# Kernel optimization log

Measured on AMD Instinct MI355X. Metric: run time of the kernel, lower is better.

Reference implementation:

```python
import jax, jax.numpy as jnp
import numpy as np

EPS = 1e-5
N_HEADS = 32
TEMPERATURE = 1.0


def _inorm(x, g, b):
    # InstanceNorm2d (affine): normalize over H,W per (N, C)
    m = jnp.mean(x, axis=(-2, -1), keepdims=True)
    v = jnp.var(x, axis=(-2, -1), keepdims=True)
    return (x - m) * jax.lax.rsqrt(v + EPS) * g + b


def _resample(x, out_hw):
    # Fourier (spectral) resampling, matching neuraloperator's resample for skips
    H, W = x.shape[-2:]
    Ho, Wo = out_hw
    if (H, W) == (Ho, Wo):
        return x
    xf = jnp.fft.rfft2(x, norm='forward')
    kh = min(H, Ho) // 2
    kw = min(W // 2 + 1, Wo // 2 + 1)
    of = jnp.zeros(x.shape[:-2] + (Ho, Wo // 2 + 1), dtype=xf.dtype)
    of = of.at[..., :kh, :kw].set(xf[..., :kh, :kw])
    of = of.at[..., -kh:, :kw].set(xf[..., -kh:, :kw])
    return jnp.fft.irfft2(of, s=(Ho, Wo), norm='forward')


def _spec_conv(x, w, out_hw):
    # w: [2(pos/neg rows), in, out, m1, m2, 2(re/im)]; fft_norm='forward'
    m1, m2 = w.shape[3], w.shape[4]
    Ho, Wo = out_hw
    wc = w[..., 0] + 1j * w[..., 1]  # [2, in, out, m1, m2]
    xf = jnp.fft.rfft2(x, norm='forward')  # [B, Cin, H, W//2+1]
    top = jnp.einsum('bimn,iomn->bomn', xf[:, :, :m1, :m2], wc[0])
    bot = jnp.einsum('bimn,iomn->bomn', xf[:, :, -m1:, :m2], wc[1])
    of = jnp.zeros((x.shape[0], w.shape[2], Ho, Wo // 2 + 1), dtype=xf.dtype)
    of = of.at[:, :, :m1, :m2].set(top)
    of = of.at[:, :, -m1:, :m2].set(bot)
    return jnp.fft.irfft2(of, s=(Ho, Wo), norm='forward')


def _fno_layer(x, w, ws, bs, out_hw, norm_gb=None, act=False):
    # one FNOBlock layer: spectral conv + linear (1x1) skip, optional instance norm + gelu
    skip = jnp.einsum('bchw,oc->bohw', x, ws) + bs[None, :, None, None]
    skip = _resample(skip, out_hw)
    fno = _spec_conv(x, w, out_hw)
    if norm_gb is not None:
        fno = _inorm(fno, norm_gb[0], norm_gb[1])
    y = fno + skip
    if act:
        y = jax.nn.gelu(y, approximate=False)  # torch F.gelu default = exact erf
    return y


def _forward(x, wK, wKs, bKs, wQ, wQs, bQs, wV, wVs, bVs, wP, wPs, bPs,
             wM0, wM0s, bM0s, wM1, wM1s, bM1s, norm_g, norm_b):
    B, T, H, W = x.shape  # token_codimension == 1 -> tokens T == channels
    xa = x.reshape(B * T, 1, H, W)
    xa_n = _inorm(xa, norm_g[0], norm_b[0])  # self.norm1
    # K, Q at half resolution (output_scaling_factor = 1/scale, scale = 2); V at full res
    k = _fno_layer(xa_n, wK, wKs, bKs, (H // 2, W // 2))
    q = _fno_layer(xa_n, wQ, wQs, bQs, (H // 2, W // 2))
    v = _fno_layer(xa_n, wV, wVs, bVs, (H, W))

    def to_seq(z):
        h, w = z.shape[-2:]
        z = z.reshape(B, T, N_HEADS, 1, h, w).transpose(0, 2, 1, 3, 4, 5)
        return z.reshape(B, N_HEADS, T, h * w)  # d = head_codim = 1

    qs, ks, vs = to_seq(q), to_seq(k), to_seq(v)
    scores = jnp.einsum('bhtd,bhsd->bhts', qs, ks) / (np.sqrt(ks.shape[-1]).astype(np.float32) * TEMPERATURE)
    attn_w = jax.nn.softmax(scores, axis=-1)
    out = jnp.einsum('bhts,bhsd->bhtd', attn_w, vs)  # [B, heads, T, H*W]
    out = out.reshape(B, N_HEADS, T, 1, H, W).transpose(0, 2, 1, 3, 4, 5)
    out = out.reshape(B * T, N_HEADS, H, W)
    # proj: n_heads*head_codim != token_codim -> FNO projection back to 1 channel
    projd = _fno_layer(out, wP, wPs, bPs, (H, W))
    attention = _inorm(projd + xa, norm_g[1], norm_b[1])  # attention_normalizer
    an = _inorm(attention, norm_g[2], norm_b[2])  # self.norm2
    # permutation-equivariant mixer: 2 FNO layers, instance_norm, gelu between layers
    m = _fno_layer(an, wM0, wM0s, bM0s, (H, W), (norm_g[3], norm_b[3]), act=True)
    m = _fno_layer(m, wM1, wM1s, bM1s, (H, W), (norm_g[4], norm_b[4]), act=False)
    output = _inorm(m, norm_g[5], norm_b[5]) + attention  # mixer_out_normalizer + residual
    return output.reshape(B, T, H, W)


def setup_inputs() -> dict:
    key = jax.random.key(0)
    ks = jax.random.split(key, 16)
    B, T, H, W, heads = 2, 32, 128, 128, 32

    def rn(k, shape, s=1.0):
        return jax.random.normal(k, shape, jnp.float32) * s

    inp = {'x': rn(ks[0], (B, T, H, W))}
    for i, nm in enumerate(['K', 'Q', 'V']):
        inp['w' + nm] = rn(ks[1 + 3 * i], (2, 1, heads, 16, 16, 2), 1.0 / heads)
        inp['w' + nm + 's'] = rn(ks[2 + 3 * i], (heads, 1), 1.0)
        inp['b' + nm + 's'] = jnp.zeros((heads,), jnp.float32)
    inp['wP'] = rn(ks[10], (2, heads, 1, 32, 32, 2), 1.0 / heads)
    inp['wPs'] = rn(ks[11], (1, heads), 1.0 / heads)
    inp['bPs'] = jnp.zeros((1,), jnp.float32)
    inp['wM0'] = rn(ks[12], (2, 1, 1, 32, 32, 2), 1.0)
    inp['wM0s'] = rn(ks[13], (1, 1), 1.0)
    inp['bM0s'] = jnp.zeros((1,), jnp.float32)
    inp['wM1'] = rn(ks[14], (2, 1, 1, 32, 32, 2), 1.0)
    inp['wM1s'] = rn(ks[15], (1, 1), 1.0)
    inp['bM1s'] = jnp.zeros((1,), jnp.float32)
    inp['norm_g'] = jnp.ones((6,), jnp.float32)
    inp['norm_b'] = jnp.zeros((6,), jnp.float32)
    return inp


def reference(x, wK, wKs, bKs, wQ, wQs, bQs, wV, wVs, bVs, wP, wPs, bPs,
              wM0, wM0s, bM0s, wM1, wM1s, bM1s, norm_g, norm_b):
    return _forward(x, wK, wKs, bKs, wQ, wQs, bQs, wV, wVs, bVs, wP, wPs, bPs,
                    wM0, wM0s, bM0s, wM1, wM1s, bM1s, norm_g, norm_b)
```

## Files before the change

kernel.cpp:

```cpp
#include <hip/hip_runtime.h>
#include <math.h>


#define EPSV 1e-5f
#define PI2 6.283185307179586f

typedef float2 cf;

__device__ __forceinline__ cf cmul(cf a, cf b){ return make_float2(a.x*b.x - a.y*b.y, a.x*b.y + a.y*b.x); }
__device__ __forceinline__ cf ldc(const float* p){ return make_float2(p[0], p[1]); }
__device__ __forceinline__ void stc(float* p, cf v){ p[0]=v.x; p[1]=v.y; }

__device__ __forceinline__ void init_tw(cf* tw, int N, float dir){
  for (int j = threadIdx.x; j < N; j += blockDim.x){
    float s, c; sincosf(dir * PI2 * (float)j / (float)N, &s, &c);
    tw[j] = make_float2(c, s);
  }
}

__device__ void breduce2(float& a, float& b){
  __shared__ float sha[16], shb[16];
  for (int off = 32; off > 0; off >>= 1){
    a += __shfl_down(a, off, 64);
    b += __shfl_down(b, off, 64);
  }
  int w = threadIdx.x >> 6, lane = threadIdx.x & 63;
  int nw = (blockDim.x + 63) >> 6;
  if (lane == 0){ sha[w] = a; shb[w] = b; }
  __syncthreads();
  if (threadIdx.x == 0){
    for (int i = 1; i < nw; ++i){ a += sha[i]; b += shb[i]; }
    sha[0] = a; shb[0] = b;
  }
  __syncthreads();
  a = sha[0]; b = shb[0];
  __syncthreads();
}

__device__ __forceinline__ cf kq_mode(const float* w, int o, int kh, int kw){
  if (kw < 16){
    if (kh < 16)  return ldc(w + ((o*16+kh)*16+kw)*2);
    if (kh >= 48) return ldc(w + (((32+o)*16+(kh-48))*16+kw)*2);
  }
  return make_float2(0.f,0.f);
}

__global__ __launch_bounds__(256) void k_gamma_xstats(
                      const float* __restrict__ wQ, const float* __restrict__ wQs,
                      const float* __restrict__ bQs,
                      const float* __restrict__ wK, const float* __restrict__ wKs,
                      const float* __restrict__ bKs,
                      const float* __restrict__ x, const float* __restrict__ ng,
                      const float* __restrict__ nb,
                      float* __restrict__ gam, float* __restrict__ gcons,
                      float* __restrict__ stats, float* __restrict__ normAB){
  if (blockIdx.x >= 32){
    int n = blockIdx.x - 32;
    const float* im = x + n*16384;
    float s=0.f, s2=0.f;
    for (int i=threadIdx.x;i<16384;i+=256){ float v=im[i]; s+=v; s2=fmaf(v,v,s2); }
    breduce2(s,s2);
    if (threadIdx.x==0){
      float m = s*(1.f/16384.f), var = s2*(1.f/16384.f)-m*m;
      float A = rsqrtf(var+EPSV)*ng[0];
      normAB[n*2]=A; normAB[n*2+1]=nb[0]-m*A;
    }
    return;
  }
  int o = blockIdx.x;
  if (o==0){ for (int i=threadIdx.x;i<640;i+=256) stats[i]=0.f; }
  float sQ=wQs[o], sK=wKs[o];
  for (int m = threadIdx.x; m < 2112; m += 256){
    int kh = m/33, kw = m-kh*33;
    cf g;
    if (kw == 0){
      int mh = (64-kh)&63;
      cf qp = kq_mode(wQ,o,kh,0);  qp.x += sQ;
      cf qm = kq_mode(wQ,o,mh,0);  qm.x += sQ;
      cf qt = make_float2(0.5f*(qp.x+qm.x), 0.5f*(qp.y-qm.y));
      cf kp = kq_mode(wK,o,kh,0);  kp.x += sK;
      cf km = kq_mode(wK,o,mh,0);  km.x += sK;
      cf kt = make_float2(0.5f*(kp.x+km.x), 0.5f*(kp.y-km.y));
      g = make_float2(64.f*(qt.x*kt.x + qt.y*kt.y), 64.f*(qt.y*kt.x - qt.x*kt.y));
    } else if (kw == 32){
      g = make_float2(64.f*sQ*sK, 0.f);
    } else {
      cf q = kq_mode(wQ,o,kh,kw); q.x += sQ;
      cf k = kq_mode(wK,o,kh,kw); k.x += sK;
      g = make_float2(128.f*(q.x*k.x + q.y*k.y), 128.f*(q.y*k.x - q.x*k.y));
    }
    stc(gam + (o*2112+m)*2, g);
  }
  if (threadIdx.x == 0){
    float qt0 = sQ + kq_mode(wQ,o,0,0).x;
    float kt0 = sK + kq_mode(wK,o,0,0).x;
    gcons[o]    = 64.f*bKs[o]*qt0;
    gcons[32+o] = 64.f*bQs[o]*kt0;
    gcons[64+o] = 64.f*bQs[o]*bKs[o];
  }
}

__global__ __launch_bounds__(256) void k_rfft_row_x(const float* __restrict__ x, const float* __restrict__ normAB,
                                                    float* __restrict__ Cw){
  __shared__ float tile[16][128];
  __shared__ cf tw[128];
  init_tw(tw, 128, -1.f);
  int n = blockIdx.x, h0 = blockIdx.y*16;
  float A = normAB[n*2], Bc = normAB[n*2+1];
  for (int i=threadIdx.x;i<2048;i+=256) tile[i>>7][i&127] = fmaf(x[n*16384 + h0*128 + i], A, Bc);
  __syncthreads();
  for (int i=threadIdx.x;i<1024;i+=256){
    int hl=i>>6, w=i&63;
    float a=tile[hl][w], b=tile[hl][w+64];
    tile[hl][w]=a+b; tile[hl][w+64]=a-b;
  }
  __syncthreads();
  int hl = threadIdx.x >> 4, kws = threadIdx.x & 15;
  for (int kw=kws; kw<33; kw+=16){
    int sel = (kw&1)? 64 : 0;
    float re=0.f, im=0.f; int idx=0;
    for (int w=0;w<64;++w){
      float v=tile[hl][sel+w]; cf t=tw[idx];
      re=fmaf(v,t.x,re); im=fmaf(v,t.y,im);
      idx=(idx+kw)&127;
    }
    float* d = Cw + (((n*128)+(h0+hl))*33 + kw)*2;
    d[0]=re*(1.f/16384.f); d[1]=im*(1.f/16384.f);
  }
}

__global__ __launch_bounds__(256) void k_fcol(const float* __restrict__ Cw, float* __restrict__ F){
  __shared__ cf col[4][128];
  __shared__ cf tw[128];
  init_tw(tw, 128, -1.f);
  int n = blockIdx.x, kwb = blockIdx.y*4;
  for (int i=threadIdx.x;i<512;i+=256){
    int kwl=i>>7, h=i&127; int kw=kwb+kwl;
    col[kwl][h] = (kw<33) ? ldc(Cw + ((n*128+h)*33+kw)*2) : make_float2(0.f,0.f);
  }
  __syncthreads();
  {
    int i = threadIdx.x;
    int kwl = i>>6, h = i&63;
    cf a = col[kwl][h], b = col[kwl][h+64];
    col[kwl][h]    = make_float2(a.x+b.x, a.y+b.y);
    col[kwl][h+64] = make_float2(a.x-b.x, a.y-b.y);
  }
  __syncthreads();
  int r = threadIdx.x & 63, kwl = threadIdx.x >> 6;
  int kw = kwb + kwl;
  if (kw >= 33) return;
  int R = (r<32)? r : r+64;
  int sel = (r&1)? 64 : 0;
  float re=0.f, im=0.f; int idx=0;
  for (int j=0;j<64;++j){
    cf v=col[kwl][sel+j]; cf t=tw[idx];
    re = fmaf(v.x,t.x,re); re = fmaf(-v.y,t.y,re);
    im = fmaf(v.x,t.y,im); im = fmaf(v.y,t.x,im);
    idx=(idx+R)&127;
  }
  stc(F + ((n*64+r)*33+kw)*2, make_float2(re,im));
}

__global__ __launch_bounds__(256) void k_score(const float* __restrict__ F, const float* __restrict__ gam,
                                               float* __restrict__ scoreP){
  __shared__ float2 Esh[66][33];
  __shared__ float2 gsh[4][66];
  int mk = blockIdx.x, b = blockIdx.y, og = blockIdx.z;
  int m0 = mk*66;
  int t = threadIdx.x >> 3, s4 = (threadIdx.x & 7) << 2;
  for (int i = threadIdx.x; i < 2112; i += 256){
    int tt = i/66, j = i - tt*66;
    int m = m0 + j;
    int kh = m/33, kw = m - kh*33;
    const float* Fb = F + (b*32+tt)*4224;
    float2 v;
    if (kw < 32) v = *(const float2*)(Fb + (kh*33+kw)*2);
    else {
      int mh = (64-kh)&63;
      float2 a = *(const float2*)(Fb + (kh*33+32)*2);
      float2 c = *(const float2*)(Fb + (mh*33+32)*2);
      v = make_float2(0.5f*(a.x+c.x), 0.5f*(a.y-c.y));
    }
    Esh[j][tt] = v;
  }
  for (int i = threadIdx.x; i < 264; i += 256){
    int ol = i/66, j = i - ol*66;
    gsh[ol][j] = *(const float2*)(gam + ((og*4+ol)*2112 + m0 + j)*2);
  }
  __syncthreads();
  float acc[4][4];
  #pragma unroll
  for (int a=0;a<4;++a) for (int k=0;k<4;++k) acc[a][k]=0.f;
  #pragma unroll 2
  for (int j=0;j<66;++j){
    float2 et = Esh[j][t];
    float2 e0 = Esh[j][s4+0];
    float2 e1 = Esh[j][s4+1];
    float2 e2 = Esh[j][s4+2];
    float2 e3 = Esh[j][s4+3];
    #pragma unroll
    for (int ol=0;ol<4;++ol){
      float2 g = gsh[ol][j];
      float a  = g.x*et.x - g.y*et.y;
      float bb = g.x*et.y + g.y*et.x;
      acc[ol][0] = fmaf(a,e0.x,fmaf(bb,e0.y,acc[ol][0]));
      acc[ol][1] = fmaf(a,e1.x,fmaf(bb,e1.y,acc[ol][1]));
      acc[ol][2] = fmaf(a,e2.x,fmaf(bb,e2.y,acc[ol][2]));
      acc[ol][3] = fmaf(a,e3.x,fmaf(bb,e3.y,acc[ol][3]));
    }
  }
  #pragma unroll
  for (int ol=0;ol<4;++ol){
    int o = og*4+ol;
    float* sp = scoreP + (((mk*2+b)*32+o)*32 + t)*32 + s4;
    sp[0]=acc[ol][0]; sp[1]=acc[ol][1]; sp[2]=acc[ol][2]; sp[3]=acc[ol][3];
  }
}

__global__ __launch_bounds__(1024) void k_softmax(float* __restrict__ attn, const float* __restrict__ F,
                                                const float* __restrict__ gcons, const float* __restrict__ scoreP){
  __shared__ float Ssh[32][33];
  int b = blockIdx.x, o = blockIdx.y;
  int t = threadIdx.x >> 5, s = threadIdx.x & 31;
  float c0=gcons[o], c1=gcons[32+o], c2=gcons[64+o];
  float sc = c0*F[(b*32+t)*4224] + c1*F[(b*32+s)*4224] + c2;
  #pragma unroll 8
  for (int p=0;p<32;++p) sc += scoreP[(((p*2+b)*32+o)*32 + t)*32 + s];
  Ssh[t][s] = sc;
  __syncthreads();
  float mx = -1e30f;
  for (int ss=0;ss<32;++ss) mx = fmaxf(mx, Ssh[t][ss]);
  float e = expf(sc - mx);
  __syncthreads();
  Ssh[t][s] = e;
  __syncthreads();
  float sum = 0.f;
  for (int ss=0;ss<32;++ss) sum += Ssh[t][ss];
  attn[(b*32+o)*1024 + t*32 + s] = e/sum;
}

__device__ __forceinline__ cf wcV_col0(const float* wV, int o, int fr){
  if (fr < 16)  return ldc(wV + ((o*16+fr)*16)*2);
  if (fr >= 112) return ldc(wV + (((32+o)*16+(fr-112))*16)*2);
  return make_float2(0.f,0.f);
}

__global__ __launch_bounds__(256) void k_pmode(const float* __restrict__ F, const float* __restrict__ attn,
                        const float* __restrict__ wV, const float* __restrict__ wVs,
                        const float* __restrict__ wP, const float* __restrict__ wPs,
                        float* __restrict__ Pm){
  __shared__ float att[32][8][32];
  __shared__ cf Fsh[32][32];
  __shared__ cf dsh[32][32];
  int b = blockIdx.x, mh = blockIdx.y, tg = blockIdx.z;
  int fr = mh<32 ? mh : mh+64;
  int half = (mh>=32)?1:0, mr = mh&31;
  for (int i=threadIdx.x; i<8192; i+=256){
    int o = i>>8, r = i&255;
    att[o][r>>5][r&31] = attn[(b*32+o)*1024 + tg*256 + r];
  }
  for (int i=threadIdx.x; i<1024; i+=256){
    int s=i>>5, kw=i&31;
    Fsh[s][kw] = ldc(F + (((b*32+s)*64+mh)*33+kw)*2);
  }
  for (int i=threadIdx.x; i<1024; i+=256){
    int o=i>>5, kw=i&31;
    cf wp = ldc(wP + (((half*32+o)*32+mr)*32+kw)*2);
    cf bP = make_float2(wPs[o]+wp.x, wp.y);
    cf aV = make_float2(wVs[o], 0.f);
    if (kw==0){
      cf w1 = wcV_col0(wV,o,fr);
      cf w2 = wcV_col0(wV,o,(128-fr)&127);
      aV.x += 0.5f*(w1.x + w2.x);
      aV.y += 0.5f*(w1.y - w2.y);
    } else if (kw<16){
      if (fr<16){ cf wv=ldc(wV + ((o*16+fr)*16+kw)*2); aV.x+=wv.x; aV.y+=wv.y; }
      else if (fr>=112){ cf wv=ldc(wV + (((32+o)*16+(fr-112))*16+kw)*2); aV.x+=wv.x; aV.y+=wv.y; }
    }
    cf c = cmul(bP, aV);
    c.x -= wPs[o]*wVs[o];
    dsh[o][kw]=c;
  }
  __syncthreads();
  int tl = threadIdx.x>>5, kw = threadIdx.x&31;
  float ax=0.f, ay=0.f;
  for (int o=0;o<32;++o){
    float er=0.f, ei=0.f;
    #pragma unroll
    for (int s4=0;s4<32;s4+=4){
      float4 a4 = *(const float4*)&att[o][tl][s4];
      cf f0=Fsh[s4][kw], f1=Fsh[s4+1][kw], f2=Fsh[s4+2][kw], f3=Fsh[s4+3][kw];
      er=fmaf(a4.x,f0.x,er); ei=fmaf(a4.x,f0.y,ei);
      er=fmaf(a4.y,f1.x,er); ei=fmaf(a4.y,f1.y,ei);
      er=fmaf(a4.z,f2.x,er); ei=fmaf(a4.z,f2.y,ei);
      er=fmaf(a4.w,f3.x,er); ei=fmaf(a4.w,f3.y,ei);
    }
    cf d = dsh[o][kw];
    ax += d.x*er - d.y*ei;
    ay += d.x*ei + d.y*er;
  }
  int t = tg*8+tl;
  stc(Pm + ((b*32+t)*2048 + mh*32+kw)*2, make_float2(ax,ay));
}

__global__ __launch_bounds__(256) void k_zmix(const float* __restrict__ x, const float* __restrict__ Pm,
                        const float* __restrict__ attn, const float* __restrict__ normAB,
                        const float* __restrict__ wVs, const float* __restrict__ wPs,
                        const float* __restrict__ wP, const float* __restrict__ bPs,
                        const float* __restrict__ bVs,
                        float* __restrict__ z, float* __restrict__ stats,
                        float* __restrict__ Tm){
  __shared__ cf Pmsh[64][33];
  __shared__ cf PmAsh[16][33];
  __shared__ float zrows[16][128];
  __shared__ float Mrow[32];
  __shared__ float cpart[33];
  __shared__ float consts;
  __shared__ cf tw[128];
  init_tw(tw, 128, 1.f);
  int n = blockIdx.x, b = n>>5, t = n&31, hb = blockIdx.y*8;
  for (int i=threadIdx.x;i<2048;i+=256)
    Pmsh[i>>5][i&31] = ldc(Pm + (n*2048 + i)*2);
  if (threadIdx.x < 32){
    int s = threadIdx.x;
    float a=0.f;
    for (int o=0;o<32;++o) a = fmaf(attn[(b*32+o)*1024 + t*32 + s], wVs[o]*wPs[o], a);
    float AxS = normAB[(b*32+s)*2], BcS = normAB[(b*32+s)*2+1];
    Mrow[s] = fmaf(a, AxS, (s==t)?1.f:0.f);
    cpart[s] = a*BcS;
  } else if (threadIdx.x == 32){
    float dcx = bPs[0];
    for (int o=0;o<32;++o){
      cf wp = ldc(wP + (o*1024)*2);
      dcx += (wPs[o]+wp.x)*bVs[o];
    }
    cpart[32] = dcx;
  }
  __syncthreads();
  if (threadIdx.x == 0){
    float c=0.f;
    for (int i=0;i<33;++i) c += cpart[i];
    consts = c;
  }
  {
    int bl = threadIdx.x>>5, kw = threadIdx.x&31;
    int h = hb + bl;
    float ser=0.f, sei=0.f, sor=0.f, soi=0.f;
    int s2h = (2*h)&127;
    int idx = 0;
    for (int khi=0;khi<32;khi+=2){
      cf v=Pmsh[khi][kw]; cf tt=tw[idx];
      ser += v.x*tt.x - v.y*tt.y; sei += v.x*tt.y + v.y*tt.x;
      idx=(idx+s2h)&127;
    }
    idx = (96*h)&127;
    for (int khi=32;khi<64;khi+=2){
      cf v=Pmsh[khi][kw]; cf tt=tw[idx];
      ser += v.x*tt.x - v.y*tt.y; sei += v.x*tt.y + v.y*tt.x;
      idx=(idx+s2h)&127;
    }
    idx = h&127;
    for (int khi=1;khi<32;khi+=2){
      cf v=Pmsh[khi][kw]; cf tt=tw[idx];
      sor += v.x*tt.x - v.y*tt.y; soi += v.x*tt.y + v.y*tt.x;
      idx=(idx+s2h)&127;
    }
    idx = (97*h)&127;
    for (int khi=33;khi<64;khi+=2){
      cf v=Pmsh[khi][kw]; cf tt=tw[idx];
      sor += v.x*tt.x - v.y*tt.y; soi += v.x*tt.y + v.y*tt.x;
      idx=(idx+s2h)&127;
    }
    PmAsh[bl][kw]   = make_float2(ser+sor, sei+soi);
    PmAsh[8+bl][kw] = make_float2(ser-sor, sei-soi);
  }
  __syncthreads();
  float cst = consts;
  float s1=0.f, s2=0.f;
  const float* xb = x + b*32*16384;
  {
    int hl = threadIdx.x>>4, wg = threadIdx.x&15;
    int w0 = wg*4;
    int gh = (hl<8)? hb+hl : hb+(hl-8)+64;
    int off = gh*128;
    float Se[4], So[4];
    #pragma unroll
    for (int j=0;j<4;++j){
      int w = w0+j;
      int s2w = (2*w)&127;
      float se=0.f, so=0.f;
      int idx=0;
      for (int kwp=0;kwp<16;++kwp){
        cf v = PmAsh[hl][2*kwp]; cf tt=tw[idx];
        float term = v.x*tt.x - v.y*tt.y;
        se += (kwp? 2.f:1.f)*term;
        idx=(idx+s2w)&127;
      }
      idx = w&127;
      for (int kwp=0;kwp<16;++kwp){
        cf v = PmAsh[hl][2*kwp+1]; cf tt=tw[idx];
        so += 2.f*(v.x*tt.x - v.y*tt.y);
        idx=(idx+s2w)&127;
      }
      Se[j]=se; So[j]=so;
    }
    float mixa[4]={0,0,0,0}, mixb[4]={0,0,0,0};
    for (int s=0;s<32;++s){
      float m = Mrow[s];
      float4 xa = *(const float4*)(xb + s*16384 + off + w0);
      float4 xc = *(const float4*)(xb + s*16384 + off + w0 + 64);
      mixa[0]=fmaf(m,xa.x,mixa[0]); mixa[1]=fmaf(m,xa.y,mixa[1]);
      mixa[2]=fmaf(m,xa.z,mixa[2]); mixa[3]=fmaf(m,xa.w,mixa[3]);
      mixb[0]=fmaf(m,xc.x,mixb[0]); mixb[1]=fmaf(m,xc.y,mixb[1]);
      mixb[2]=fmaf(m,xc.z,mixb[2]); mixb[3]=fmaf(m,xc.w,mixb[3]);
    }
    float oa[4], ob[4];
    #pragma unroll
    for (int j=0;j<4;++j){
      oa[j] = cst + Se[j] + So[j] + mixa[j];
      ob[j] = cst + Se[j] - So[j] + mixb[j];
      s1 += oa[j]+ob[j];
      s2 += oa[j]*oa[j] + ob[j]*ob[j];
      zrows[hl][w0+j]    = oa[j];
      zrows[hl][w0+64+j] = ob[j];
    }
    *(float4*)(z + n*16384 + off + w0)      = make_float4(oa[0],oa[1],oa[2],oa[3]);
    *(float4*)(z + n*16384 + off + w0 + 64) = make_float4(ob[0],ob[1],ob[2],ob[3]);
  }
  __syncthreads();
  for (int i=threadIdx.x;i<1024;i+=256){
    int hl=i>>6, w=i&63;
    float a=zrows[hl][w], bz=zrows[hl][w+64];
    zrows[hl][w]=a+bz; zrows[hl][w+64]=a-bz;
  }
  __syncthreads();
  for (int i=threadIdx.x;i<512;i+=256){
    int hl=i>>5, kw=i&31;
    int gh = (hl<8)? hb+hl : hb+(hl-8)+64;
    int sel = (kw&1)? 64 : 0;
    float re=0.f, im=0.f; int idx=0;
    for (int w=0;w<64;++w){
      float v=zrows[hl][sel+w]; cf tt=tw[idx];
      re=fmaf(v,tt.x,re); im=fmaf(v,tt.y,im);
      idx=(idx+kw)&127;
    }
    float* d = Tm + ((n*128+gh)*32+kw)*2;
    d[0]=re*(1.f/16384.f); d[1]=-im*(1.f/16384.f);
  }
  breduce2(s1,s2);
  if (threadIdx.x==0){ atomicAdd(&stats[n*2],s1); atomicAdd(&stats[n*2+1],s2); }
}

__global__ __launch_bounds__(256) void k_colpair(const float* __restrict__ Tm, const float* __restrict__ wM,
                                                 const float* __restrict__ statsZ,
                                                 const float* __restrict__ ng, const float* __restrict__ nb,
                                                 int apply_an, float* __restrict__ Am){
  __shared__ cf Tsh[128][9];
  __shared__ cf Gsh[64][9];
  __shared__ cf tw[128];
  init_tw(tw,128,-1.f);
  int n = blockIdx.x, kw8 = blockIdx.y*8;
  float C1 = 1.f, Dc128 = 0.f;
  if (apply_an){
    float S=statsZ[n*2], S2=statsZ[n*2+1];
    float mz=S*(1.f/16384.f), vz=S2*(1.f/16384.f)-mz*mz;
    float az=rsqrtf(vz+EPSV);
    float g1=ng[1], g2=ng[2];
    float vat = g1*g1*vz*az*az;
    C1 = az*g1*rsqrtf(vat+EPSV)*g2;
    Dc128 = (nb[2] - mz*C1)*(1.f/128.f);
  }
  for (int i=threadIdx.x;i<1024;i+=256){
    int h=i>>3, kwl=i&7;
    cf v = ldc(Tm + ((n*128+h)*32 + kw8+kwl)*2);
    v.x *= C1; v.y *= C1;
    if (apply_an && (kw8+kwl)==0) v.x += Dc128;
    Tsh[h][kwl] = v;
  }
  __syncthreads();
  for (int i=threadIdx.x;i<512;i+=256){
    int h=i>>3, kwl=i&7;
    cf a=Tsh[h][kwl], b=Tsh[h+64][kwl];
    Tsh[h][kwl]    = make_float2(a.x+b.x, a.y+b.y);
    Tsh[h+64][kwl] = make_float2(a.x-b.x, a.y-b.y);
  }
  __syncthreads();
  {
    int kwl = threadIdx.x&7, base = threadIdx.x>>3;
    for (int r=0;r<2;++r){
      int khi = r*32 + base;
      int khF = (khi<32)? khi : khi+64;
      int sel = (khi&1)? 64 : 0;
      float re=0.f, im=0.f; int idx=0;
      for (int j=0;j<64;++j){
        cf v=Tsh[sel+j][kwl]; cf t=tw[idx];
        re += v.x*t.x - v.y*t.y; im += v.x*t.y + v.y*t.x;
        idx=(idx+khF)&127;
      }
      int half=(khi>=32)?1:0, mr=khi&31;
      cf wv = ldc(wM + ((half*32+mr)*32 + kw8+kwl)*2);
      Gsh[khi][kwl] = cmul(make_float2(re,im), wv);
    }
  }
  __syncthreads();
  {
    int kwl = threadIdx.x&7, base = threadIdx.x>>3;
    for (int r=0;r<2;++r){
      int h = r*32 + base;
      float ser=0.f, sei=0.f, sor=0.f, soi=0.f;
      int s2h = (2*h)&127;
      int idx=0;
      for (int khi=0;khi<32;khi+=2){
        cf v=Gsh[khi][kwl]; cf t=tw[idx];
        ser += v.x*t.x + v.y*t.y; sei += v.y*t.x - v.x*t.y;
        idx=(idx+s2h)&127;
      }
      idx=(96*h)&127;
      for (int khi=32;khi<64;khi+=2){
        cf v=Gsh[khi][kwl]; cf t=tw[idx];
        ser += v.x*t.x + v.y*t.y; sei += v.y*t.x - v.x*t.y;
        idx=(idx+s2h)&127;
      }
      idx=h&127;
      for (int khi=1;khi<32;khi+=2){
        cf v=Gsh[khi][kwl]; cf t=tw[idx];
        sor += v.x*t.x + v.y*t.y; soi += v.y*t.x - v.x*t.y;
        idx=(idx+s2h)&127;
      }
      idx=(97*h)&127;
      for (int khi=33;khi<64;khi+=2){
        cf v=Gsh[khi][kwl]; cf t=tw[idx];
        sor += v.x*t.x + v.y*t.y; soi += v.y*t.x - v.x*t.y;
        idx=(idx+s2h)&127;
      }
      stc(Am + ((n*128+h)*32 + kw8+kwl)*2,    make_float2(ser+sor, sei+soi));
      stc(Am + ((n*128+h+64)*32 + kw8+kwl)*2, make_float2(ser-sor, sei-soi));
    }
  }
}

__global__ __launch_bounds__(256) void k_mirfft_row(const float* __restrict__ Am, float* __restrict__ out,
                                                    float* __restrict__ stats,
                                                    const float* __restrict__ m0, float* __restrict__ statsC,
                                                    int withCross){
  __shared__ cf rowA[16][33];
  __shared__ cf tw[128];
  init_tw(tw,128,1.f);
  int n=blockIdx.x, h0=blockIdx.y*16;
  for (int i=threadIdx.x;i<512;i+=256){
    int hl=i>>5, kw=i&31;
    rowA[hl][kw] = ldc(Am + ((n*128+h0+hl)*32+kw)*2);
  }
  __syncthreads();
  float s=0.f,s2=0.f,s3=0.f;
  for (int i=threadIdx.x;i<1024;i+=256){
    int hl=i>>6, w=i&63;
    int s2w = (2*w)&127;
    float se=0.f, so=0.f;
    int idx=0;
    for (int kwp=0;kwp<16;++kwp){
      cf v=rowA[hl][2*kwp]; cf t=tw[idx];
      float term=v.x*t.x-v.y*t.y;
      se += (kwp? 2.f:1.f)*term;
      idx=(idx+s2w)&127;
    }
    idx = w&127;
    for (int kwp=0;kwp<16;++kwp){
      cf v=rowA[hl][2*kwp+1]; cf t=tw[idx];
      so += 2.f*(v.x*t.x-v.y*t.y);
      idx=(idx+s2w)&127;
    }
    float oa = se+so, ob = se-so;
    int gi = n*16384+(h0+hl)*128+w;
    out[gi]    = oa;
    out[gi+64] = ob;
    s+=oa+ob; s2 += oa*oa + ob*ob;
    if (withCross){
      s3 = fmaf(oa, m0[gi], s3);
      s3 = fmaf(ob, m0[gi+64], s3);
    }
  }
  breduce2(s,s2);
  if (threadIdx.x==0){ atomicAdd(&stats[n*2],s); atomicAdd(&stats[n*2+1],s2); }
  if (withCross){
    float d=0.f;
    breduce2(s3,d);
    if (threadIdx.x==0) atomicAdd(&statsC[n*2],s3);
  }
}

__global__ __launch_bounds__(256) void k_m0_rfft_row(const float* __restrict__ fno, const float* __restrict__ z,
                              const float* __restrict__ stats0, const float* __restrict__ statsZ,
                              const float* __restrict__ ng, const float* __restrict__ nb,
                              const float* __restrict__ wM0s, const float* __restrict__ bM0s,
                              float* __restrict__ m0out, float* __restrict__ Tm,
                              float* __restrict__ statsM0){
  __shared__ float tile[16][128];
  __shared__ cf tw[128];
  init_tw(tw,128,-1.f);
  int n=blockIdx.x, h0=blockIdx.y*16;
  float S0=stats0[n*2], S02=stats0[n*2+1];
  float m0m=S0*(1.f/16384.f), v0=S02*(1.f/16384.f)-m0m*m0m;
  float A0=rsqrtf(v0+EPSV)*ng[3];
  float B0=nb[3]-m0m*A0;
  float Sz=statsZ[n*2], Sz2=statsZ[n*2+1];
  float mz=Sz*(1.f/16384.f), vz=Sz2*(1.f/16384.f)-mz*mz;
  float az=rsqrtf(vz+EPSV);
  float g1=ng[1], g2=ng[2];
  float vat=g1*g1*vz*az*az;
  float C1=az*g1*rsqrtf(vat+EPSV)*g2;
  float Dc=nb[2]-mz*C1;
  float ws_=wM0s[0], bs_=bM0s[0];
  float sm=0.f, sm2=0.f;
  for (int i=threadIdx.x;i<2048;i+=256){
    int gi = n*16384 + h0*128 + i;
    float nf = fmaf(fno[gi], A0, B0);
    float an = fmaf(z[gi], C1, Dc);
    float pre = nf + fmaf(ws_, an, bs_);
    float gv = 0.5f*pre*(1.f+erff(pre*0.70710678118654752f));
    tile[i>>7][i&127]=gv;
    m0out[gi]=gv;
    sm+=gv; sm2=fmaf(gv,gv,sm2);
  }
  __syncthreads();
  for (int i=threadIdx.x;i<1024;i+=256){
    int hl=i>>6, w=i&63;
    float a=tile[hl][w], b=tile[hl][w+64];
    tile[hl][w]=a+b; tile[hl][w+64]=a-b;
  }
  __syncthreads();
  for (int i=threadIdx.x;i<512;i+=256){
    int hl=i>>5, kw=i&31;
    int sel = (kw&1)? 64:0;
    float re=0.f,im=0.f; int idx=0;
    for (int w=0;w<64;++w){
      float v=tile[hl][sel+w]; cf t=tw[idx];
      re=fmaf(v,t.x,re); im=fmaf(v,t.y,im);
      idx=(idx+kw)&127;
    }
    float* d = Tm + ((n*128+h0+hl)*32+kw)*2;
    d[0]=re*(1.f/16384.f); d[1]=im*(1.f/16384.f);
  }
  breduce2(sm,sm2);
  if (threadIdx.x==0){ atomicAdd(&statsM0[n*2],sm); atomicAdd(&statsM0[n*2+1],sm2); }
}

__global__ __launch_bounds__(256) void k_final(const float* __restrict__ f1, const float* __restrict__ m0,
                        const float* __restrict__ z,
                        const float* __restrict__ stats1, const float* __restrict__ statsM0,
                        const float* __restrict__ statsC, const float* __restrict__ statsZ,
                        const float* __restrict__ ng, const float* __restrict__ nb,
                        const float* __restrict__ wM1s, const float* __restrict__ bM1s,
                        float* __restrict__ out){
  int n=blockIdx.x, h0=blockIdx.y*16;
  const float N = 16384.f, iN = 1.f/16384.f;
  float Sf=stats1[n*2], Sf2=stats1[n*2+1];
  float m1m=Sf*iN, v1=Sf2*iN-m1m*m1m;
  float A1=rsqrtf(v1+EPSV)*ng[4];
  float Bc1=nb[4]-m1m*A1;
  float ws_=wM1s[0], K=Bc1+bM1s[0];
  float Sm=statsM0[n*2], Sm2=statsM0[n*2+1], Sfm=statsC[n*2];
  float S1m = A1*Sf + ws_*Sm + N*K;
  float S2m = A1*A1*Sf2 + ws_*ws_*Sm2 + N*K*K + 2.f*A1*ws_*Sfm + 2.f*A1*K*Sf + 2.f*ws_*K*Sm;
  float mean2 = S1m*iN, var2 = S2m*iN - mean2*mean2;
  float A2=rsqrtf(var2+EPSV)*ng[5];
  float B2c=nb[5]-mean2*A2;
  float Sz=statsZ[n*2], Sz2=statsZ[n*2+1];
  float mz=Sz*iN, vz=Sz2*iN-mz*mz;
  float Az=rsqrtf(vz+EPSV)*ng[1];
  float Bz=nb[1]-mz*Az;
  float cf1 = A2*A1, cm0 = A2*ws_, cc = A2*K + B2c;
  for (int i=threadIdx.x;i<2048;i+=256){
    int gi=n*16384+h0*128+i;
    out[gi] = fmaf(f1[gi],cf1, fmaf(m0[gi],cm0, cc)) + fmaf(z[gi],Az,Bz);
  }
}

extern "C" void kernel_launch(void* const* d_in, const int* in_sizes, int n_in,
                              void* d_out, int out_size, void* d_ws, size_t ws_size,
                              hipStream_t stream){
  (void)in_sizes; (void)n_in; (void)out_size; (void)ws_size;
  const float* x   = (const float*)d_in[0];
  const float* wK  = (const float*)d_in[1];
  const float* wKs = (const float*)d_in[2];
  const float* bKs = (const float*)d_in[3];
  const float* wQ  = (const float*)d_in[4];
  const float* wQs = (const float*)d_in[5];
  const float* bQs = (const float*)d_in[6];
  const float* wV  = (const float*)d_in[7];
  const float* wVs = (const float*)d_in[8];
  const float* bVs = (const float*)d_in[9];
  const float* wP  = (const float*)d_in[10];
  const float* wPs = (const float*)d_in[11];
  const float* bPs = (const float*)d_in[12];
  const float* wM0 = (const float*)d_in[13];
  const float* wM0s= (const float*)d_in[14];
  const float* bM0s= (const float*)d_in[15];
  const float* wM1 = (const float*)d_in[16];
  const float* wM1s= (const float*)d_in[17];
  const float* bM1s= (const float*)d_in[18];
  const float* ng  = (const float*)d_in[19];
  const float* nb  = (const float*)d_in[20];
  float* out = (float*)d_out;
  float* ws  = (float*)d_ws;

  float* F      = ws;
  float* Cw     = F + 270336;
  float* scoreP = Cw + 540672;
  float* attn   = scoreP + 2097152;
  float* stats  = attn + 65536;
  float* Pm     = stats + 640;
  float* gcons  = Pm + 262144;
  float* gam    = gcons + 128;
  float* normAB = gam + 135168;
  float* z      = normAB + 128;
  float* m0b    = z + 1048576;
  float* fx     = m0b + 1048576;
  float* Tm     = fx + 1048576;
  float* Am     = Tm + 524288;
  float* statsZ = stats;
  float* stats0 = stats + 128;
  float* stats1 = stats + 256;
  float* statsM0= stats + 384;
  float* statsC = stats + 512;

  k_gamma_xstats<<<96,256,0,stream>>>(wQ,wQs,bQs, wK,wKs,bKs, x, ng, nb, gam, gcons, stats, normAB);
  k_rfft_row_x<<<dim3(64,8),256,0,stream>>>(x, normAB, Cw);
  k_fcol<<<dim3(64,9),256,0,stream>>>(Cw, F);
  k_score<<<dim3(32,2,8),256,0,stream>>>(F, gam, scoreP);
  k_softmax<<<dim3(2,32),1024,0,stream>>>(attn, F, gcons, scoreP);
  k_pmode<<<dim3(2,64,4),256,0,stream>>>(F, attn, wV, wVs, wP, wPs, Pm);
  k_zmix<<<dim3(64,8),256,0,stream>>>(x, Pm, attn, normAB, wVs, wPs, wP, bPs, bVs, z, statsZ, Tm);
  k_colpair<<<dim3(64,4),256,0,stream>>>(Tm, wM0, statsZ, ng, nb, 1, Am);
  k_mirfft_row<<<dim3(64,8),256,0,stream>>>(Am, fx, stats0, (const float*)nullptr, (float*)nullptr, 0);
  k_m0_rfft_row<<<dim3(64,8),256,0,stream>>>(fx, z, stats0, statsZ, ng, nb, wM0s, bM0s, m0b, Tm, statsM0);
  k_colpair<<<dim3(64,4),256,0,stream>>>(Tm, wM1, statsZ, ng, nb, 0, Am);
  k_mirfft_row<<<dim3(64,8),256,0,stream>>>(Am, fx, stats1, m0b, statsC, 1);
  k_final<<<dim3(64,8),256,0,stream>>>(fx, m0b, z, stats1, statsM0, statsC, statsZ, ng, nb, wM1s, bM1s, out);
}
```

Before: 250.7 us.

## Compute norm stats in spectral domain and fuse inverse row FFTs into consumers

The spatial-domain sum and sum-of-squares (plus the cross term) needed for instance norm are now computed from the spectral coefficients inside k_colpair using Parseval's identity. That removes the need to materialize the inverse-FFT output before the stats are known. The inverse row DFT is then fused into the GELU/m0 kernel and into the final combine kernel, cutting two launches and one full-size intermediate buffer round-trip. The cost is extra Parseval bookkeeping with subtle edge cases (DC and Nyquist columns, mirrored rows), and the sign convention of Tm's imaginary part changes, which makes correctness fragile.

After: 235.4 us, median of 2. 1.07x faster.

```diff
diff --git a/kernel.cpp b/kernel.cpp
--- a/kernel.cpp
+++ b/kernel.cpp
@@ -455,9 +455,12 @@
 __global__ __launch_bounds__(256) void k_colpair(const float* __restrict__ Tm, const float* __restrict__ wM,
                                                  const float* __restrict__ statsZ,
                                                  const float* __restrict__ ng, const float* __restrict__ nb,
-                                                 int apply_an, float* __restrict__ Am){
+                                                 int apply_an, float* __restrict__ Am,
+                                                 float* __restrict__ statsF,
+                                                 float* __restrict__ statsC, int do_cross){
   __shared__ cf Tsh[128][9];
   __shared__ cf Gsh[64][9];
+  __shared__ cf Msh[64][9];
   __shared__ cf tw[128];
   init_tw(tw,128,-1.f);
   int n = blockIdx.x, kw8 = blockIdx.y*8;
@@ -500,6 +503,7 @@
       }
       int half=(khi>=32)?1:0, mr=khi&31;
       cf wv = ldc(wM + ((half*32+mr)*32 + kw8+kwl)*2);
+      Msh[khi][kwl] = make_float2(re,im);
       Gsh[khi][kwl] = cmul(make_float2(re,im), wv);
     }
   }
@@ -538,13 +542,60 @@
       stc(Am + ((n*128+h+64)*32 + kw8+kwl)*2, make_float2(ser-sor, sei-soi));
     }
   }
-}
-
-__global__ __launch_bounds__(256) void k_mirfft_row(const float* __restrict__ Am, float* __restrict__ out,
-                                                    float* __restrict__ stats,
-                                                    const float* __restrict__ m0, float* __restrict__ statsC,
-                                                    int withCross){
+  float p2=0.f, cx=0.f;
+  for (int i=threadIdx.x;i<512;i+=256){
+    int khi=i>>3, kwl=i&7;
+    int kw=kw8+kwl;
+    if (kw>=1){
+      cf g=Gsh[khi][kwl];
+      p2 += 2.f*(g.x*g.x+g.y*g.y);
+      if (do_cross){ cf m=Msh[khi][kwl]; cx += 2.f*(g.x*m.x+g.y*m.y); }
+    }
+  }
+  if (kw8==0){
+    int tid=threadIdx.x;
+    if (tid==0){
+      cf g0=Gsh[0][0];
+      p2 += g0.x*g0.x;
+      if (do_cross) cx += g0.x*Msh[0][0].x;
+      atomicAdd(&statsF[n*2], 16384.f*g0.x);
+    } else if (tid<32){
+      cf a=Gsh[tid][0], b=Gsh[64-tid][0];
+      float fex=0.5f*(a.x+b.x), fey=0.5f*(a.y-b.y);
+      p2 += 2.f*(fex*fex+fey*fey);
+      if (do_cross){ cf m=Msh[tid][0]; cx += 2.f*(fex*m.x+fey*m.y); }
+    } else if (tid==32){
+      cf v=Gsh[32][0];
+      p2 += 0.5f*(v.x*v.x+v.y*v.y);
+      if (do_cross){
+        float mr=0.f, mi=0.f;
+        for (int j=0;j<64;++j){
+          cf u=Tsh[j][0];
+          int q=j&3;
+          if (q==0){ mr+=u.x; mi+=u.y; }
+          else if (q==1){ mr+=u.y; mi-=u.x; }
+          else if (q==2){ mr-=u.x; mi-=u.y; }
+          else        { mr-=u.y; mi+=u.x; }
+        }
+        cx += v.x*mr + v.y*mi;
+      }
+    }
+  }
+  breduce2(p2,cx);
+  if (threadIdx.x==0){
+    atomicAdd(&statsF[n*2+1], 16384.f*p2);
+    if (do_cross) atomicAdd(&statsC[n*2], 16384.f*cx);
+  }
+}
+
+__global__ __launch_bounds__(256) void k_m0_irow(const float* __restrict__ Am, const float* __restrict__ z,
+                              const float* __restrict__ stats0, const float* __restrict__ statsZ,
+                              const float* __restrict__ ng, const float* __restrict__ nb,
+                              const float* __restrict__ wM0s, const float* __restrict__ bM0s,
+                              float* __restrict__ m0out, float* __restrict__ Tm,
+                              float* __restrict__ statsM0){
   __shared__ cf rowA[16][33];
+  __shared__ float tile[16][128];
   __shared__ cf tw[128];
   init_tw(tw,128,1.f);
   int n=blockIdx.x, h0=blockIdx.y*16;
@@ -552,54 +603,6 @@
     int hl=i>>5, kw=i&31;
     rowA[hl][kw] = ldc(Am + ((n*128+h0+hl)*32+kw)*2);
   }
-  __syncthreads();
-  float s=0.f,s2=0.f,s3=0.f;
-  for (int i=threadIdx.x;i<1024;i+=256){
-    int hl=i>>6, w=i&63;
-    int s2w = (2*w)&127;
-    float se=0.f, so=0.f;
-    int idx=0;
-    for (int kwp=0;kwp<16;++kwp){
-      cf v=rowA[hl][2*kwp]; cf t=tw[idx];
-      float term=v.x*t.x-v.y*t.y;
-      se += (kwp? 2.f:1.f)*term;
-      idx=(idx+s2w)&127;
-    }
-    idx = w&127;
-    for (int kwp=0;kwp<16;++kwp){
-      cf v=rowA[hl][2*kwp+1]; cf t=tw[idx];
-      so += 2.f*(v.x*t.x-v.y*t.y);
-      idx=(idx+s2w)&127;
-    }
-    float oa = se+so, ob = se-so;
-    int gi = n*16384+(h0+hl)*128+w;
-    out[gi]    = oa;
-    out[gi+64] = ob;
-    s+=oa+ob; s2 += oa*oa + ob*ob;
-    if (withCross){
-      s3 = fmaf(oa, m0[gi], s3);
-      s3 = fmaf(ob, m0[gi+64], s3);
-    }
-  }
-  breduce2(s,s2);
-  if (threadIdx.x==0){ atomicAdd(&stats[n*2],s); atomicAdd(&stats[n*2+1],s2); }
-  if (withCross){
-    float d=0.f;
-    breduce2(s3,d);
-    if (threadIdx.x==0) atomicAdd(&statsC[n*2],s3);
-  }
-}
-
-__global__ __launch_bounds__(256) void k_m0_rfft_row(const float* __restrict__ fno, const float* __restrict__ z,
-                              const float* __restrict__ stats0, const float* __restrict__ statsZ,
-                              const float* __restrict__ ng, const float* __restrict__ nb,
-                              const float* __restrict__ wM0s, const float* __restrict__ bM0s,
-                              float* __restrict__ m0out, float* __restrict__ Tm,
-                              float* __restrict__ statsM0){
-  __shared__ float tile[16][128];
-  __shared__ cf tw[128];
-  init_tw(tw,128,-1.f);
-  int n=blockIdx.x, h0=blockIdx.y*16;
   float S0=stats0[n*2], S02=stats0[n*2+1];
   float m0m=S0*(1.f/16384.f), v0=S02*(1.f/16384.f)-m0m*m0m;
   float A0=rsqrtf(v0+EPSV)*ng[3];
@@ -612,16 +615,36 @@
   float C1=az*g1*rsqrtf(vat+EPSV)*g2;
   float Dc=nb[2]-mz*C1;
   float ws_=wM0s[0], bs_=bM0s[0];
+  __syncthreads();
   float sm=0.f, sm2=0.f;
-  for (int i=threadIdx.x;i<2048;i+=256){
-    int gi = n*16384 + h0*128 + i;
-    float nf = fmaf(fno[gi], A0, B0);
-    float an = fmaf(z[gi], C1, Dc);
-    float pre = nf + fmaf(ws_, an, bs_);
-    float gv = 0.5f*pre*(1.f+erff(pre*0.70710678118654752f));
-    tile[i>>7][i&127]=gv;
-    m0out[gi]=gv;
-    sm+=gv; sm2=fmaf(gv,gv,sm2);
+  for (int i=threadIdx.x;i<1024;i+=256){
+    int hl=i>>6, w=i&63;
+    int s2w = (2*w)&127;
+    float se=0.f, so=0.f;
+    int idx=0;
+    for (int kwp=0;kwp<16;++kwp){
+      cf v=rowA[hl][2*kwp]; cf t=tw[idx];
+      float term=v.x*t.x-v.y*t.y;
+      se += (kwp? 2.f:1.f)*term;
+      idx=(idx+s2w)&127;
+    }
+    idx = w&127;
+    for (int kwp=0;kwp<16;++kwp){
+      cf v=rowA[hl][2*kwp+1]; cf t=tw[idx];
+      so += 2.f*(v.x*t.x-v.y*t.y);
+      idx=(idx+s2w)&127;
+    }
+    float oa = se+so, ob = se-so;
+    int gi = n*16384+(h0+hl)*128+w;
+    float an_a = fmaf(z[gi],C1,Dc);
+    float pre_a = fmaf(oa,A0,B0) + fmaf(ws_,an_a,bs_);
+    float ga = 0.5f*pre_a*(1.f+erff(pre_a*0.70710678118654752f));
+    m0out[gi]=ga; tile[hl][w]=ga;
+    float an_b = fmaf(z[gi+64],C1,Dc);
+    float pre_b = fmaf(ob,A0,B0) + fmaf(ws_,an_b,bs_);
+    float gb = 0.5f*pre_b*(1.f+erff(pre_b*0.70710678118654752f));
+    m0out[gi+64]=gb; tile[hl][w+64]=gb;
+    sm += ga+gb; sm2 += ga*ga + gb*gb;
   }
   __syncthreads();
   for (int i=threadIdx.x;i<1024;i+=256){
@@ -640,20 +663,27 @@
       idx=(idx+kw)&127;
     }
     float* d = Tm + ((n*128+h0+hl)*32+kw)*2;
-    d[0]=re*(1.f/16384.f); d[1]=im*(1.f/16384.f);
+    d[0]=re*(1.f/16384.f); d[1]=-im*(1.f/16384.f);
   }
   breduce2(sm,sm2);
   if (threadIdx.x==0){ atomicAdd(&statsM0[n*2],sm); atomicAdd(&statsM0[n*2+1],sm2); }
 }
 
-__global__ __launch_bounds__(256) void k_final(const float* __restrict__ f1, const float* __restrict__ m0,
+__global__ __launch_bounds__(256) void k_final_irow(const float* __restrict__ Am, const float* __restrict__ m0,
                         const float* __restrict__ z,
                         const float* __restrict__ stats1, const float* __restrict__ statsM0,
                         const float* __restrict__ statsC, const float* __restrict__ statsZ,
                         const float* __restrict__ ng, const float* __restrict__ nb,
                         const float* __restrict__ wM1s, const float* __restrict__ bM1s,
                         float* __restrict__ out){
+  __shared__ cf rowA[16][33];
+  __shared__ cf tw[128];
+  init_tw(tw,128,1.f);
   int n=blockIdx.x, h0=blockIdx.y*16;
+  for (int i=threadIdx.x;i<512;i+=256){
+    int hl=i>>5, kw=i&31;
+    rowA[hl][kw] = ldc(Am + ((n*128+h0+hl)*32+kw)*2);
+  }
   const float N = 16384.f, iN = 1.f/16384.f;
   float Sf=stats1[n*2], Sf2=stats1[n*2+1];
   float m1m=Sf*iN, v1=Sf2*iN-m1m*m1m;
@@ -671,9 +701,28 @@
   float Az=rsqrtf(vz+EPSV)*ng[1];
   float Bz=nb[1]-mz*Az;
   float cf1 = A2*A1, cm0 = A2*ws_, cc = A2*K + B2c;
-  for (int i=threadIdx.x;i<2048;i+=256){
-    int gi=n*16384+h0*128+i;
-    out[gi] = fmaf(f1[gi],cf1, fmaf(m0[gi],cm0, cc)) + fmaf(z[gi],Az,Bz);
+  __syncthreads();
+  for (int i=threadIdx.x;i<1024;i+=256){
+    int hl=i>>6, w=i&63;
+    int s2w = (2*w)&127;
+    float se=0.f, so=0.f;
+    int idx=0;
+    for (int kwp=0;kwp<16;++kwp){
+      cf v=rowA[hl][2*kwp]; cf t=tw[idx];
+      float term=v.x*t.x-v.y*t.y;
+      se += (kwp? 2.f:1.f)*term;
+      idx=(idx+s2w)&127;
+    }
+    idx = w&127;
+    for (int kwp=0;kwp<16;++kwp){
+      cf v=rowA[hl][2*kwp+1]; cf t=tw[idx];
+      so += 2.f*(v.x*t.x-v.y*t.y);
+      idx=(idx+s2w)&127;
+    }
+    float oa = se+so, ob = se-so;
+    int gi = n*16384+(h0+hl)*128+w;
+    out[gi]    = fmaf(oa,cf1, fmaf(m0[gi],cm0, cc)) + fmaf(z[gi],Az,Bz);
+    out[gi+64] = fmaf(ob,cf1, fmaf(m0[gi+64],cm0, cc)) + fmaf(z[gi+64],Az,Bz);
   }
 }
 
@@ -716,8 +765,7 @@
   float* normAB = gam + 135168;
   float* z      = normAB + 128;
   float* m0b    = z + 1048576;
-  float* fx     = m0b + 1048576;
-  float* Tm     = fx + 1048576;
+  float* Tm     = m0b + 1048576;
   float* Am     = Tm + 524288;
   float* statsZ = stats;
   float* stats0 = stats + 128;
@@ -732,10 +780,8 @@
   k_softmax<<<dim3(2,32),1024,0,stream>>>(attn, F, gcons, scoreP);
   k_pmode<<<dim3(2,64,4),256,0,stream>>>(F, attn, wV, wVs, wP, wPs, Pm);
   k_zmix<<<dim3(64,8),256,0,stream>>>(x, Pm, attn, normAB, wVs, wPs, wP, bPs, bVs, z, statsZ, Tm);
-  k_colpair<<<dim3(64,4),256,0,stream>>>(Tm, wM0, statsZ, ng, nb, 1, Am);
-  k_mirfft_row<<<dim3(64,8),256,0,stream>>>(Am, fx, stats0, (const float*)nullptr, (float*)nullptr, 0);
-  k_m0_rfft_row<<<dim3(64,8),256,0,stream>>>(fx, z, stats0, statsZ, ng, nb, wM0s, bM0s, m0b, Tm, statsM0);
-  k_colpair<<<dim3(64,4),256,0,stream>>>(Tm, wM1, statsZ, ng, nb, 0, Am);
-  k_mirfft_row<<<dim3(64,8),256,0,stream>>>(Am, fx, stats1, m0b, statsC, 1);
-  k_final<<<dim3(64,8),256,0,stream>>>(fx, m0b, z, stats1, statsM0, statsC, statsZ, ng, nb, wM1s, bM1s, out);
-}
+  k_colpair<<<dim3(64,4),256,0,stream>>>(Tm, wM0, statsZ, ng, nb, 1, Am, stats0, (float*)nullptr, 0);
+  k_m0_irow<<<dim3(64,8),256,0,stream>>>(Am, z, stats0, statsZ, ng, nb, wM0s, bM0s, m0b, Tm, statsM0);
+  k_colpair<<<dim3(64,4),256,0,stream>>>(Tm, wM1, statsZ, ng, nb, 0, Am, stats1, statsC, 1);
+  k_final_irow<<<dim3(64,8),256,0,stream>>>(Am, m0b, z, stats1, statsM0, statsC, statsZ, ng, nb, wM1s, bM1s, out);
+}
```
